# Optimization experiments

Measured on AMD Instinct MI355X. Metric: run time of the kernel, lower is better.

## Reference

```python
import jax, jax.numpy as jnp
import numpy as np

BS, HEADS, H, W, DIM = 2, 8, 64, 64, 32

def setup_inputs() -> dict:
    key = jax.random.key(0)
    ks = jax.random.split(key, 5)
    shape = (BS, HEADS, H, W, DIM)
    return {
        "q": jax.random.normal(ks[0], shape, dtype=jnp.float32),
        "k": jax.random.normal(ks[1], shape, dtype=jnp.float32),
        "v": jax.random.normal(ks[2], shape, dtype=jnp.float32),
        "emb_h": jax.random.normal(ks[3], (H, DIM), dtype=jnp.float32),
        "emb_w": jax.random.normal(ks[4], (W, DIM), dtype=jnp.float32),
    }

def reference(q, k, v, emb_h, emb_w):
    bs, heads, h, w, dim = q.shape
    q = q * (dim ** -0.5)
    # content logits: [bs, heads, h, w, h, w]
    logits = jnp.einsum('bnhwd,bnpqd->bnhwpq', q, k)
    # absolute positional logits: emb[p,q,d] = emb_h[p,d] + emb_w[q,d]
    emb = emb_h[:, None, :] + emb_w[None, :, :]
    logits = logits + jnp.einsum('bnxyd,pqd->bnxypq', q, emb)
    weights = jax.nn.softmax(logits.reshape(bs, heads, h, w, h * w), axis=-1)
    weights = weights.reshape(bs, heads, h, w, h, w)
    attn_out = jnp.einsum('bnhwpq,bnpqd->bhwnd', weights, v)
    # fold_heads=True
    return attn_out.reshape(bs, h, w, heads * dim)
```

## Files before the change

kernel.cpp:

```cpp
#include <hip/hip_runtime.h>
#include <math.h>


#define BATCH 2
#define NHEAD 8
#define NBH   (BATCH * NHEAD)
#define DIM   32
#define SEQ   4096
#define KT    32
#define NW    4
#define KPW   (SEQ / NW)
#define QPB   64
#define NG    4
#define TILES (KPW / KT)
#define NTILE (SEQ / KT)
#define CDW   21
#define VSTR  68

typedef short short8 __attribute__((ext_vector_type(8)));
typedef float f32x4  __attribute__((ext_vector_type(4)));
typedef int   int4v  __attribute__((ext_vector_type(4)));

static __device__ inline float fast_exp2(float x) {
#if __has_builtin(__builtin_amdgcn_exp2f)
    return __builtin_amdgcn_exp2f(x);
#else
    return exp2f(x);
#endif
}
static __device__ inline unsigned pk_rhu(float a, float b) {
    unsigned ua = __builtin_bit_cast(unsigned, a) + 0x8000u;
    unsigned ub = __builtin_bit_cast(unsigned, b) + 0x8000u;
#if __has_builtin(__builtin_amdgcn_perm)
    return __builtin_amdgcn_perm(ub, ua, 0x07060302u);
#else
    return (ua >> 16) | (ub & 0xffff0000u);
#endif
}
static __device__ inline unsigned pk_trunc(float a, float b) {
    unsigned ua = __builtin_bit_cast(unsigned, a);
    unsigned ub = __builtin_bit_cast(unsigned, b);
#if __has_builtin(__builtin_amdgcn_perm)
    return __builtin_amdgcn_perm(ub, ua, 0x07060302u);
#else
    return (ua >> 16) | (ub & 0xffff0000u);
#endif
}
static __device__ inline unsigned short bf_rhu(float a) {
    return (unsigned short)((__builtin_bit_cast(unsigned, a) + 0x8000u) >> 16);
}

__global__ __launch_bounds__(256) void prep_kernel(
    const float* __restrict__ k,
    const float* __restrict__ v,
    const float* __restrict__ emb_h,
    const float* __restrict__ emb_w,
    unsigned short* __restrict__ K2,
    unsigned short* __restrict__ VH)
{
    __shared__ unsigned short vt[DIM][VSTR];

    const int blk    = blockIdx.x;
    const int bn     = blk >> 6;
    const int keyblk = blk & 63;
    const int kl     = threadIdx.x >> 2;
    const int oct    = threadIdx.x & 3;
    const int key    = (keyblk << 6) + kl;

    const float* kr = k + ((size_t)bn * SEQ + key) * DIM + oct * 8;
    float4 k0 = ((const float4*)kr)[0], k1 = ((const float4*)kr)[1];
    const float* eh = emb_h + (key >> 6) * DIM + oct * 8;
    float4 e0 = ((const float4*)eh)[0], e1 = ((const float4*)eh)[1];
    const float* ew = emb_w + (key & 63) * DIM + oct * 8;
    float4 f0 = ((const float4*)ew)[0], f1 = ((const float4*)ew)[1];
    k0.x += e0.x + f0.x; k0.y += e0.y + f0.y; k0.z += e0.z + f0.z; k0.w += e0.w + f0.w;
    k1.x += e1.x + f1.x; k1.y += e1.y + f1.y; k1.z += e1.z + f1.z; k1.w += e1.w + f1.w;
    int4v kw;
    kw[0] = (int)pk_rhu(k0.x, k0.y); kw[1] = (int)pk_rhu(k0.z, k0.w);
    kw[2] = (int)pk_rhu(k1.x, k1.y); kw[3] = (int)pk_rhu(k1.z, k1.w);
    *(int4v*)(K2 + ((size_t)bn * SEQ + key) * DIM + oct * 8) = kw;

    const int loc = kl & 31;
    const int pos = (kl & 32) + ((loc & 15) >> 2) * 8 + (loc & 3) + ((loc >> 4) & 1) * 4;
    const float* vr = v + ((size_t)bn * SEQ + key) * DIM + oct * 8;
    float4 v0 = ((const float4*)vr)[0], v1 = ((const float4*)vr)[1];
    float vv[8] = { v0.x, v0.y, v0.z, v0.w, v1.x, v1.y, v1.z, v1.w };
#pragma unroll
    for (int i = 0; i < 8; i++)
        vt[oct * 8 + i][pos] = bf_rhu(vv[i]);
    __syncthreads();

    const int d = threadIdx.x >> 3;
    const int c = threadIdx.x & 7;
    unsigned long long r0 = *(const unsigned long long*)&vt[d][c * 8];
    unsigned long long r1 = *(const unsigned long long*)&vt[d][c * 8 + 4];
    unsigned short* dst = VH
        + (((size_t)bn * NTILE + keyblk * 2 + (c >> 2)) * DIM + d) * KT
        + (c & 3) * 8;
    *(unsigned long long*)(dst)     = r0;
    *(unsigned long long*)(dst + 4) = r1;
}

__global__ __launch_bounds__(256, 4) void attn_kernel(
    const float* __restrict__ q,
    const unsigned short* __restrict__ K2,
    const unsigned short* __restrict__ VH,
    float* __restrict__ out)
{
    __shared__ unsigned comb[NW][64][CDW];

    const int lin  = blockIdx.x;
    const int xcd  = lin & 7;
    const int ii   = lin >> 3;
    const int bn   = (xcd << 1) | (ii >> 6);
    const int qblk = ii & 63;
    const int b    = bn >> 3;
    const int n    = bn & 7;

    const int tid  = threadIdx.x;
    const int w    = tid >> 6;
    const int ln   = tid & 63;
    const int l16  = ln & 15;
    const int quad = ln >> 4;
    const int qbase = qblk * QPB;
    const float SC = 0.25503472251093478f;

    short8 qh[NG];
#pragma unroll
    for (int g = 0; g < NG; g++) {
        const int qrow = qbase + g * 16 + l16;
        const float4* qp = (const float4*)(q + ((size_t)bn * SEQ + qrow) * DIM + quad * 8);
        float4 qa = qp[0], qb = qp[1];
        int4v hi4;
        hi4[0] = (int)pk_rhu(qa.x * SC, qa.y * SC);
        hi4[1] = (int)pk_rhu(qa.z * SC, qa.w * SC);
        hi4[2] = (int)pk_rhu(qb.x * SC, qb.y * SC);
        hi4[3] = (int)pk_rhu(qb.z * SC, qb.w * SC);
        qh[g] = __builtin_bit_cast(short8, hi4);
    }

    int4v ones4;
    ones4[0] = 0x3F803F80; ones4[1] = 0x3F803F80;
    ones4[2] = 0x3F803F80; ones4[3] = 0x3F803F80;
    const short8 aone = __builtin_bit_cast(short8, ones4);

    f32x4 o[NG][2];
    f32x4 lacc[NG];
#pragma unroll
    for (int g = 0; g < NG; g++) {
        o[g][0] = (f32x4){0,0,0,0};
        o[g][1] = (f32x4){0,0,0,0};
        lacc[g] = (f32x4){0,0,0,0};
    }

    const unsigned short* kptr  = K2 + (size_t)bn * SEQ * DIM + ((size_t)(w * KPW + l16)) * DIM + quad * 8;
    const unsigned short* vptr0 = VH + ((size_t)bn * NTILE + w * TILES) * (DIM * KT)
                                     + (size_t)l16 * KT + quad * 8;
    const unsigned short* vptr1 = vptr0 + 16 * KT;

    short8 a0 = *(const short8*)kptr;
    short8 a1 = *(const short8*)(kptr + 16 * DIM);

    for (int t = 0; t < TILES; t++) {
        short8 h0 = *(const short8*)vptr0;
        short8 h1 = *(const short8*)vptr1;
        vptr0 += KT * DIM; vptr1 += KT * DIM;

        short8 a0n = a0, a1n = a1;
        if (t + 1 < TILES) {
            kptr += KT * DIM;
            a0n = *(const short8*)kptr;
            a1n = *(const short8*)(kptr + 16 * DIM);
        }

#pragma unroll
        for (int g = 0; g < NG; g++) {
            f32x4 s0 = __builtin_amdgcn_mfma_f32_16x16x32_bf16(a0, qh[g], (f32x4){0,0,0,0}, 0, 0, 0);
            f32x4 s1 = __builtin_amdgcn_mfma_f32_16x16x32_bf16(a1, qh[g], (f32x4){0,0,0,0}, 0, 0, 0);

            float p0[4], p1[4];
#pragma unroll
            for (int r = 0; r < 4; r++) {
                p0[r] = fast_exp2(s0[r]);
                p1[r] = fast_exp2(s1[r]);
            }

            int4v pp;
            pp[0] = (int)pk_trunc(p0[0], p0[1]); pp[1] = (int)pk_trunc(p0[2], p0[3]);
            pp[2] = (int)pk_trunc(p1[0], p1[1]); pp[3] = (int)pk_trunc(p1[2], p1[3]);
            short8 bp = __builtin_bit_cast(short8, pp);

            lacc[g] = __builtin_amdgcn_mfma_f32_16x16x32_bf16(aone, bp, lacc[g], 0, 0, 0);

            o[g][0] = __builtin_amdgcn_mfma_f32_16x16x32_bf16(h0, bp, o[g][0], 0, 0, 0);
            o[g][1] = __builtin_amdgcn_mfma_f32_16x16x32_bf16(h1, bp, o[g][1], 0, 0, 0);
        }

        a0 = a0n; a1 = a1n;
    }

    __syncthreads();
    {
        unsigned* my = &comb[w][ln][0];
#pragma unroll
        for (int g = 0; g < NG; g++) {
#pragma unroll
            for (int h = 0; h < 2; h++) {
                my[g * 4 + h * 2 + 0] = pk_rhu(o[g][h][0], o[g][h][1]);
                my[g * 4 + h * 2 + 1] = pk_rhu(o[g][h][2], o[g][h][3]);
            }
            my[16 + g] = __builtin_bit_cast(unsigned, lacc[g][0]);
        }
    }
    __syncthreads();

    {
        const int qlc  = tid >> 2;
        const int dblk = tid & 3;
        const int g    = qlc >> 4;
        const int ll   = qlc & 15;
        float lt = 0.f;
#pragma unroll
        for (int w4 = 0; w4 < NW; w4++)
            lt += __builtin_bit_cast(float, comb[w4][ll][16 + g]);
        const float inv = 1.0f / lt;
        float res[8];
#pragma unroll
        for (int dd = 0; dd < 8; dd++) res[dd] = 0.f;
#pragma unroll
        for (int w4 = 0; w4 < NW; w4++) {
#pragma unroll
            for (int dd = 0; dd < 8; dd++) {
                const int d    = dblk * 8 + dd;
                const int h    = d >> 4;
                const int qd   = (d >> 2) & 3;
                const int pr   = (d & 3) >> 1;
                const int half = d & 1;
                unsigned pw = comb[w4][qd * 16 + ll][g * 4 + h * 2 + pr];
                unsigned bits = half ? (pw & 0xffff0000u) : (pw << 16);
                res[dd] += __builtin_bit_cast(float, bits);
            }
        }
        float* op = out + ((size_t)(b * SEQ + qbase + qlc)) * (NHEAD * DIM) + n * DIM + dblk * 8;
        ((float4*)op)[0] = (float4){ res[0] * inv, res[1] * inv, res[2] * inv, res[3] * inv };
        ((float4*)op)[1] = (float4){ res[4] * inv, res[5] * inv, res[6] * inv, res[7] * inv };
    }
}

extern "C" void kernel_launch(void* const* d_in, const int* in_sizes, int n_in,
                              void* d_out, int out_size, void* d_ws, size_t ws_size,
                              hipStream_t stream) {
    const float* q     = (const float*)d_in[0];
    const float* k     = (const float*)d_in[1];
    const float* v     = (const float*)d_in[2];
    const float* emb_h = (const float*)d_in[3];
    const float* emb_w = (const float*)d_in[4];
    float* out = (float*)d_out;

    unsigned short* K2 = (unsigned short*)d_ws;
    unsigned short* VH = K2 + (size_t)NBH * SEQ * DIM;

    prep_kernel<<<dim3(NBH * (SEQ / 64)), dim3(256), 0, stream>>>(k, v, emb_h, emb_w, K2, VH);
    attn_kernel<<<dim3(NBH * (SEQ / QPB)), dim3(256), 0, stream>>>(q, K2, VH, out);
}
```

Measured before the change: 121.1 us.

## Software-pipeline PV MFMAs one tile behind and replace ones-MFMA row sum

```diff
diff --git a/kernel.cpp b/kernel.cpp
--- a/kernel.cpp
+++ b/kernel.cpp
@@ -46,6 +46,9 @@
     return (ua >> 16) | (ub & 0xffff0000u);
 #endif
 }
+static __device__ inline float tr_bf16(float x) {
+    return __builtin_bit_cast(float, __builtin_bit_cast(unsigned, x) & 0xffff0000u);
+}
 static __device__ inline unsigned short bf_rhu(float a) {
     return (unsigned short)((__builtin_bit_cast(unsigned, a) + 0x8000u) >> 16);
 }
@@ -139,64 +142,80 @@
         qh[g] = __builtin_bit_cast(short8, hi4);
     }
 
-    int4v ones4;
-    ones4[0] = 0x3F803F80; ones4[1] = 0x3F803F80;
-    ones4[2] = 0x3F803F80; ones4[3] = 0x3F803F80;
-    const short8 aone = __builtin_bit_cast(short8, ones4);
-
     f32x4 o[NG][2];
-    f32x4 lacc[NG];
+    float lsum[NG];
 #pragma unroll
     for (int g = 0; g < NG; g++) {
         o[g][0] = (f32x4){0,0,0,0};
         o[g][1] = (f32x4){0,0,0,0};
-        lacc[g] = (f32x4){0,0,0,0};
+        lsum[g] = 0.f;
     }
 
     const unsigned short* kptr  = K2 + (size_t)bn * SEQ * DIM + ((size_t)(w * KPW + l16)) * DIM + quad * 8;
     const unsigned short* vptr0 = VH + ((size_t)bn * NTILE + w * TILES) * (DIM * KT)
                                      + (size_t)l16 * KT + quad * 8;
-    const unsigned short* vptr1 = vptr0 + 16 * KT;
 
     short8 a0 = *(const short8*)kptr;
     short8 a1 = *(const short8*)(kptr + 16 * DIM);
-
-    for (int t = 0; t < TILES; t++) {
-        short8 h0 = *(const short8*)vptr0;
-        short8 h1 = *(const short8*)vptr1;
-        vptr0 += KT * DIM; vptr1 += KT * DIM;
-
-        short8 a0n = a0, a1n = a1;
-        if (t + 1 < TILES) {
-            kptr += KT * DIM;
-            a0n = *(const short8*)kptr;
-            a1n = *(const short8*)(kptr + 16 * DIM);
-        }
+    short8 h0 = *(const short8*)vptr0;
+    short8 h1 = *(const short8*)(vptr0 + 16 * KT);
+    vptr0 += KT * DIM;
+
+    short8 bp[NG];
+#pragma unroll
+    for (int g = 0; g < NG; g++) {
+        f32x4 s0 = __builtin_amdgcn_mfma_f32_16x16x32_bf16(a0, qh[g], (f32x4){0,0,0,0}, 0, 0, 0);
+        f32x4 s1 = __builtin_amdgcn_mfma_f32_16x16x32_bf16(a1, qh[g], (f32x4){0,0,0,0}, 0, 0, 0);
+        float p0[4], p1[4];
+#pragma unroll
+        for (int r = 0; r < 4; r++) { p0[r] = fast_exp2(s0[r]); p1[r] = fast_exp2(s1[r]); }
+        lsum[g] += ((tr_bf16(p0[0]) + tr_bf16(p0[1])) + (tr_bf16(p0[2]) + tr_bf16(p0[3])))
+                 + ((tr_bf16(p1[0]) + tr_bf16(p1[1])) + (tr_bf16(p1[2]) + tr_bf16(p1[3])));
+        int4v pp;
+        pp[0] = (int)pk_trunc(p0[0], p0[1]); pp[1] = (int)pk_trunc(p0[2], p0[3]);
+        pp[2] = (int)pk_trunc(p1[0], p1[1]); pp[3] = (int)pk_trunc(p1[2], p1[3]);
+        bp[g] = __builtin_bit_cast(short8, pp);
+    }
+    kptr += KT * DIM;
+    a0 = *(const short8*)kptr;
+    a1 = *(const short8*)(kptr + 16 * DIM);
+
+    for (int t = 1; t < TILES; t++) {
+        short8 h0n = *(const short8*)vptr0;
+        short8 h1n = *(const short8*)(vptr0 + 16 * KT);
+        vptr0 += KT * DIM;
+        kptr += KT * DIM;
+        short8 a0n = *(const short8*)kptr;
+        short8 a1n = *(const short8*)(kptr + 16 * DIM);
 
 #pragma unroll
         for (int g = 0; g < NG; g++) {
             f32x4 s0 = __builtin_amdgcn_mfma_f32_16x16x32_bf16(a0, qh[g], (f32x4){0,0,0,0}, 0, 0, 0);
             f32x4 s1 = __builtin_amdgcn_mfma_f32_16x16x32_bf16(a1, qh[g], (f32x4){0,0,0,0}, 0, 0, 0);
 
+            o[g][0] = __builtin_amdgcn_mfma_f32_16x16x32_bf16(h0, bp[g], o[g][0], 0, 0, 0);
+            o[g][1] = __builtin_amdgcn_mfma_f32_16x16x32_bf16(h1, bp[g], o[g][1], 0, 0, 0);
+
             float p0[4], p1[4];
 #pragma unroll
-            for (int r = 0; r < 4; r++) {
-                p0[r] = fast_exp2(s0[r]);
-                p1[r] = fast_exp2(s1[r]);
-            }
+            for (int r = 0; r < 4; r++) { p0[r] = fast_exp2(s0[r]); p1[r] = fast_exp2(s1[r]); }
+
+            lsum[g] += ((tr_bf16(p0[0]) + tr_bf16(p0[1])) + (tr_bf16(p0[2]) + tr_bf16(p0[3])))
+                     + ((tr_bf16(p1[0]) + tr_bf16(p1[1])) + (tr_bf16(p1[2]) + tr_bf16(p1[3])));
 
             int4v pp;
             pp[0] = (int)pk_trunc(p0[0], p0[1]); pp[1] = (int)pk_trunc(p0[2], p0[3]);
             pp[2] = (int)pk_trunc(p1[0], p1[1]); pp[3] = (int)pk_trunc(p1[2], p1[3]);
-            short8 bp = __builtin_bit_cast(short8, pp);
-
-            lacc[g] = __builtin_amdgcn_mfma_f32_16x16x32_bf16(aone, bp, lacc[g], 0, 0, 0);
-
-            o[g][0] = __builtin_amdgcn_mfma_f32_16x16x32_bf16(h0, bp, o[g][0], 0, 0, 0);
-            o[g][1] = __builtin_amdgcn_mfma_f32_16x16x32_bf16(h1, bp, o[g][1], 0, 0, 0);
+            bp[g] = __builtin_bit_cast(short8, pp);
         }
 
-        a0 = a0n; a1 = a1n;
+        h0 = h0n; h1 = h1n; a0 = a0n; a1 = a1n;
+    }
+
+#pragma unroll
+    for (int g = 0; g < NG; g++) {
+        o[g][0] = __builtin_amdgcn_mfma_f32_16x16x32_bf16(h0, bp[g], o[g][0], 0, 0, 0);
+        o[g][1] = __builtin_amdgcn_mfma_f32_16x16x32_bf16(h1, bp[g], o[g][1], 0, 0, 0);
     }
 
     __syncthreads();
@@ -209,7 +228,7 @@
                 my[g * 4 + h * 2 + 0] = pk_rhu(o[g][h][0], o[g][h][1]);
                 my[g * 4 + h * 2 + 1] = pk_rhu(o[g][h][2], o[g][h][3]);
             }
-            my[16 + g] = __builtin_bit_cast(unsigned, lacc[g][0]);
+            my[16 + g] = __builtin_bit_cast(unsigned, lsum[g]);
         }
     }
     __syncthreads();
@@ -222,7 +241,9 @@
         float lt = 0.f;
 #pragma unroll
         for (int w4 = 0; w4 < NW; w4++)
-            lt += __builtin_bit_cast(float, comb[w4][ll][16 + g]);
+#pragma unroll
+            for (int qu = 0; qu < 4; qu++)
+                lt += __builtin_bit_cast(float, comb[w4][qu * 16 + ll][16 + g]);
         const float inv = 1.0f / lt;
         float res[8];
 #pragma unroll
```

New measurement: 128.9 us. 6.5% more time.
